# Kernel optimization log

Hardware: AMD Instinct MI355X
Metric: run time of the kernel (lower is better)

## Reference

```python
import jax, jax.numpy as jnp
import numpy as np

NUM_USERS = 100000
NUM_ITEMS = 50000
EMB = 64
N_SOC = 1000000
N_RAT = 1000000
BATCH = 16384
EPS = 1e-8


def setup_inputs() -> dict:
    key = jax.random.key(0)
    ks = jax.random.split(key, 8)
    user_emb = 0.01 * jax.random.normal(ks[0], (NUM_USERS, EMB), jnp.float32)
    item_emb = 0.01 * jax.random.normal(ks[1], (NUM_ITEMS, EMB), jnp.float32)
    users = jax.random.randint(ks[2], (BATCH,), 0, NUM_USERS)
    items = jax.random.randint(ks[3], (BATCH,), 0, NUM_ITEMS)
    social_src = jax.random.randint(ks[4], (N_SOC,), 0, NUM_USERS)
    social_dst = jax.random.randint(ks[5], (N_SOC,), 0, NUM_USERS)
    like_u = jax.random.randint(ks[6], (N_RAT,), 0, NUM_USERS)
    like_i = jax.random.randint(ks[7], (N_RAT,), 0, NUM_ITEMS)
    return {"user_emb": user_emb, "item_emb": item_emb, "users": users,
            "items": items, "social_src": social_src, "social_dst": social_dst,
            "like_u": like_u, "like_i": like_i}


def _deg(idx, num):
    # node degree as float column vector [num, 1]
    return jax.ops.segment_sum(jnp.ones((idx.shape[0],), jnp.float32), idx,
                               num_segments=num)[:, None]


def _seg_mean(msg, idx, num):
    s = jax.ops.segment_sum(msg, idx, num_segments=num)
    cnt = _deg(idx, num)
    return s / jnp.maximum(cnt, 1.0)


def reference(user_emb, item_emb, users, items, social_src, social_dst, like_u, like_i):
    # degree-based self-weights (deg=0 -> 1, deg>0 -> ~0)
    user_deg = _deg(like_u, NUM_USERS)            # out-degree on 'like'
    u_sw = 1.0 - user_deg / (user_deg + EPS)
    item_deg = _deg(like_i, NUM_ITEMS)            # out-degree on 'rev_like'
    i_sw = 1.0 - item_deg / (item_deg + EPS)

    def social_conv(hu):
        # mean aggregation over user->user social edges
        return _seg_mean(hu[social_src], social_dst, NUM_USERS)

    def rating_conv(hu, hi):
        # user <- mean of liked-item embeddings, plus degree-gated self
        new_u = u_sw * hu + _seg_mean(hi[like_i], like_u, NUM_USERS)
        new_i = i_sw * hi + _seg_mean(hu[like_u], like_i, NUM_ITEMS)
        return new_u, new_i

    # layer 1
    soc1 = social_conv(user_emb)
    rat_u1, rat_i1 = rating_conv(user_emb, item_emb)
    u1 = 0.5 * soc1 + 0.5 * rat_u1
    # layer 2 (stacked on per-branch states, as in the torch code)
    soc2 = social_conv(soc1)
    rat_u2, _ = rating_conv(rat_u1, rat_i1)
    u2 = 0.5 * soc2 + 0.5 * rat_u2

    # l_user = [0, 1, 2]
    final_user = user_emb + u1 + u2
    final_item = item_emb

    latest_user = final_user[users]
    latest_item = final_item[items]
    predict = jax.nn.sigmoid(jnp.sum(latest_user * latest_item, axis=1))
    return predict, latest_user, latest_item
```

## Files before the change

### kernel.cpp

```cpp
#include <hip/hip_runtime.h>
#include <hip/hip_bf16.h>

#define NUSERS 100000
#define NITEMS 50000
#define NEDGE  1000000
#define NBATCH 16384
#define CAP_LU 320000
#define EPB    2048
#define NBLK_E ((NEDGE + EPB - 1) / EPB)
#define NBW    3125

#define OFF_GC     0
#define OFF_GB     768
#define OFF_GCUR   1536
#define OFF_BITS   2304
#define OFF_NEED   (OFF_BITS + 3136)
#define OFF_ZEND   (OFF_NEED + NUSERS / 4)
#define OFF_IDEG   OFF_ZEND
#define OFF_UDEG   (OFF_IDEG + NITEMS)
#define OFF_SDEG   (OFF_UDEG + NUSERS)
#define OFF_ISTART (OFF_SDEG + NUSERS)
#define OFF_USTART (OFF_ISTART + NITEMS)
#define OFF_SSTART (OFF_USTART + NUSERS)
#define OFF_PARTLI (OFF_SSTART + NUSERS)
#define OFF_PARTLU (OFF_PARTLI + NEDGE)
#define OFF_PARTSD (OFF_PARTLU + CAP_LU)
#define OFF_UEMBH  OFF_PARTLI
#define OFF_CSRLI  (OFF_UEMBH + NUSERS * 32)
#define OFF_CSRLU  (OFF_CSRLI + NEDGE)
#define OFF_RI1    (OFF_CSRLU + CAP_LU)
#define OFF_SOC1   OFF_CSRLI
#define OFF_CSRSD  (OFF_SOC1 + NUSERS * 32)
#define OFF_RU1C   (OFF_CSRSD + NEDGE)
#define OFF_RU2C   (OFF_RU1C + NBATCH * 32)
#define WS_FLOATS  (OFF_RU2C + NBATCH * 32)

typedef unsigned short u16;

__device__ __forceinline__ float bf2f(u16 h) {
    union { unsigned u; float f; } c; c.u = ((unsigned)h) << 16; return c.f;
}
__device__ __forceinline__ u16 f2bf(float f) {
    union { float f; unsigned u; } c; c.f = f;
    unsigned r = c.u + 0x7fffu + ((c.u >> 16) & 1u);
    return (u16)(r >> 16);
}
__device__ __forceinline__ void acc2(unsigned w, float& a0, float& a1) {
    a0 += bf2f((u16)(w & 0xffff));
    a1 += bf2f((u16)(w >> 16));
}

__global__ void k_slot(const int* __restrict__ users, unsigned* __restrict__ bits,
                       unsigned char* __restrict__ needed) {
    int b = blockIdx.x * blockDim.x + threadIdx.x;
    if (b < NBATCH) {
        int u = users[b];
        atomicOr(&bits[u >> 5], 1u << (u & 31));
        needed[u] = 1;
    }
}

__global__ void k_passA(const int* __restrict__ lu, const int* __restrict__ li,
                        const int* __restrict__ sd, const int* __restrict__ ss,
                        const unsigned* __restrict__ bits, int* __restrict__ gcnt,
                        unsigned char* __restrict__ needed) {
    __shared__ int lc[768];
    __shared__ unsigned sbits[NBW];
    int t = threadIdx.x;
    for (int k = t; k < 768; k += 256) lc[k] = 0;
    for (int k = t; k < NBW; k += 256) sbits[k] = bits[k];
    __syncthreads();
    int base = blockIdx.x * EPB;
    int end = base + EPB; if (end > NEDGE) end = NEDGE;
    for (int e = base + t; e < end; e += 256) {
        int item = li[e], a = lu[e], d = sd[e];
        atomicAdd(&lc[item >> 9], 1);
        if ((sbits[a >> 5] >> (a & 31)) & 1)
            atomicAdd(&lc[256 + (a >> 9)], 1);
        atomicAdd(&lc[512 + (d >> 9)], 1);
        if ((sbits[d >> 5] >> (d & 31)) & 1)
            needed[ss[e]] = 1;
    }
    __syncthreads();
    for (int k = t; k < 768; k += 256)
        if (lc[k]) atomicAdd(&gcnt[k], lc[k]);
}

__global__ void k_passB(const int* __restrict__ gcnt, int* __restrict__ gbase,
                        int* __restrict__ gcur) {
    __shared__ int s[256];
    int t = threadIdx.x;
    for (int j = 0; j < 3; ++j) {
        int v = gcnt[j * 256 + t];
        s[t] = v;
        __syncthreads();
        for (int o = 1; o < 256; o <<= 1) {
            int x = (t >= o) ? s[t - o] : 0;
            __syncthreads();
            s[t] += x;
            __syncthreads();
        }
        int ex = s[t] - v;
        gbase[j * 256 + t] = ex;
        gcur[j * 256 + t] = ex;
        __syncthreads();
    }
}

__global__ void k_passC(const int* __restrict__ lu, const int* __restrict__ li,
                        const int* __restrict__ sd, const int* __restrict__ ss,
                        const unsigned* __restrict__ bits, int* __restrict__ gcur,
                        int* __restrict__ partLI, int* __restrict__ partLU,
                        int* __restrict__ partSD) {
    __shared__ int lc[768];
    __shared__ int go[768];
    __shared__ unsigned sbits[NBW];
    int t = threadIdx.x;
    for (int k = t; k < 768; k += 256) lc[k] = 0;
    for (int k = t; k < NBW; k += 256) sbits[k] = bits[k];
    __syncthreads();
    int base = blockIdx.x * EPB;
    int end = base + EPB; if (end > NEDGE) end = NEDGE;
    unsigned mask = 0;
    int i = 0;
    for (int e = base + t; e < end; e += 256, ++i) {
        int item = li[e], a = lu[e], d = sd[e];
        atomicAdd(&lc[item >> 9], 1);
        if ((sbits[a >> 5] >> (a & 31)) & 1) {
            atomicAdd(&lc[256 + (a >> 9)], 1);
            mask |= (1u << i);
        }
        atomicAdd(&lc[512 + (d >> 9)], 1);
    }
    __syncthreads();
    for (int k = t; k < 768; k += 256) {
        go[k] = lc[k] ? atomicAdd(&gcur[k], lc[k]) : 0;
        lc[k] = 0;
    }
    __syncthreads();
    i = 0;
    for (int e = base + t; e < end; e += 256, ++i) {
        int item = li[e], a = lu[e], d = sd[e], s_ = ss[e];
        int b0 = item >> 9;
        int r0 = atomicAdd(&lc[b0], 1);
        partLI[go[b0] + r0] = (a << 9) | (item & 511);
        if (mask & (1u << i)) {
            int b1 = 256 + (a >> 9);
            int r1 = atomicAdd(&lc[b1], 1);
            partLU[go[b1] + r1] = (item << 9) | (a & 511);
        }
        int b2 = 512 + (d >> 9);
        int r2 = atomicAdd(&lc[b2], 1);
        partSD[go[b2] + r2] = (s_ << 9) | (d & 511);
    }
}

__global__ void k_passD(const int* __restrict__ gcnt, const int* __restrict__ gbase,
                        const int* __restrict__ partLI, const int* __restrict__ partLU,
                        const int* __restrict__ partSD, int* __restrict__ csrli,
                        int* __restrict__ csrlu, int* __restrict__ csrsd,
                        int* __restrict__ ideg, int* __restrict__ udeg,
                        int* __restrict__ sdeg, int* __restrict__ istart,
                        int* __restrict__ ustart, int* __restrict__ sstart) {
    __shared__ int lcnt[512], lstart[512], sb[2][512];
    int t = threadIdx.x;
    int blk = blockIdx.x, list, b;
    const int* part; int* csr; int* deg; int* start; int n;
    if (blk < 196)      { list = 0; b = blk;       part = partLI; csr = csrli; deg = ideg; start = istart; n = NITEMS; }
    else if (blk < 392) { list = 1; b = blk - 196; part = partLU; csr = csrlu; deg = udeg; start = ustart; n = NUSERS; }
    else                { list = 2; b = blk - 392; part = partSD; csr = csrsd; deg = sdeg; start = sstart; n = NUSERS; }
    int base = gbase[list * 256 + b], cnt = gcnt[list * 256 + b];
    int node0 = b << 9;
    int M = n - node0; if (M > 512) M = 512; if (M < 0) M = 0;

    lcnt[t] = 0; lcnt[t + 256] = 0;
    __syncthreads();
    for (int i = t; i < cnt; i += 256) atomicAdd(&lcnt[part[base + i] & 511], 1);
    __syncthreads();
    sb[0][t] = lcnt[t]; sb[0][t + 256] = lcnt[t + 256];
    __syncthreads();
    int pp = 0;
    for (int o = 1; o < 512; o <<= 1) {
        int np = pp ^ 1;
        for (int k = t; k < 512; k += 256) {
            int v = sb[pp][k];
            if (k >= o) v += sb[pp][k - o];
            sb[np][k] = v;
        }
        __syncthreads();
        pp = np;
    }
    for (int k = t; k < 512; k += 256) {
        int ex = sb[pp][k] - lcnt[k];
        lstart[k] = ex;
        if (k < M) { deg[node0 + k] = lcnt[k]; start[node0 + k] = base + ex; }
    }
    __syncthreads();
    lcnt[t] = 0; lcnt[t + 256] = 0;
    __syncthreads();
    for (int i = t; i < cnt; i += 256) {
        int p = part[base + i];
        int nl = p & 511;
        int r = atomicAdd(&lcnt[nl], 1);
        csr[base + lstart[nl] + r] = p >> 9;
    }
}

__global__ void k_cvt(const float* __restrict__ src, u16* __restrict__ dst) {
    int t = blockIdx.x * 256 + threadIdx.x;
    if (t >= NUSERS * 16) return;
    float4 v = ((const float4*)src)[t];
    ushort4 o;
    o.x = f2bf(v.x); o.y = f2bf(v.y); o.z = f2bf(v.z); o.w = f2bf(v.w);
    ((ushort4*)dst)[t] = o;
}

__global__ void k_gather_item(const float* __restrict__ iemb,
                              const unsigned* __restrict__ uh32,
                              const int* __restrict__ csr, const int* __restrict__ istart,
                              const int* __restrict__ ideg, unsigned* __restrict__ ri1) {
    int node = blockIdx.x * 4 + (threadIdx.x >> 6);
    int lane = threadIdx.x & 63;
    if (node >= NITEMS) return;
    int half = lane >> 5, l = lane & 31;
    int j = istart[node], dg = ideg[node], end = j + dg;
    float a0 = 0.f, b0 = 0.f, a1 = 0.f, b1 = 0.f, a2 = 0.f, b2 = 0.f, a3 = 0.f, b3 = 0.f;
    for (; j + 7 < end; j += 8) {
        unsigned w0 = uh32[csr[j     + half] * 32 + l];
        unsigned w1 = uh32[csr[j + 2 + half] * 32 + l];
        unsigned w2 = uh32[csr[j + 4 + half] * 32 + l];
        unsigned w3 = uh32[csr[j + 6 + half] * 32 + l];
        acc2(w0, a0, b0); acc2(w1, a1, b1); acc2(w2, a2, b2); acc2(w3, a3, b3);
    }
    for (; j < end; j += 2) {
        int idx = j + half;
        if (idx < end) { unsigned w = uh32[csr[idx] * 32 + l]; acc2(w, a0, b0); }
    }
    float s0 = (a0 + a1) + (a2 + a3);
    float s1 = (b0 + b1) + (b2 + b3);
    s0 += __shfl_xor(s0, 32);
    s1 += __shfl_xor(s1, 32);
    if (half == 0) {
        float dgf = (float)dg;
        float inv = 1.0f / fmaxf(dgf, 1.0f);
        float sw = 1.0f - dgf / (dgf + 1e-8f);
        float2 ev = ((const float2*)(iemb + node * 64))[l];
        float v0 = sw * ev.x + s0 * inv;
        float v1 = sw * ev.y + s1 * inv;
        ri1[node * 32 + l] = (unsigned)f2bf(v0) | ((unsigned)f2bf(v1) << 16);
    }
}

__global__ void k_batch_rat(const int* __restrict__ users, const float* __restrict__ iemb,
                            const u16* __restrict__ ri1, const int* __restrict__ csr,
                            const int* __restrict__ ustart, const int* __restrict__ udeg,
                            u16* __restrict__ ru1c, u16* __restrict__ ru2c) {
    int b = blockIdx.x * 4 + (threadIdx.x >> 6);
    int lane = threadIdx.x & 63;
    if (b >= NBATCH) return;
    int u = users[b];
    int j = ustart[u], dg = udeg[u], end = j + dg;
    float a1 = 0.f, a2 = 0.f, b1 = 0.f, b2 = 0.f;
    for (; j + 1 < end; j += 2) {
        int i0 = csr[j], i1 = csr[j + 1];
        a1 += iemb[i0 * 64 + lane];
        b1 += iemb[i1 * 64 + lane];
        a2 += bf2f(ri1[i0 * 64 + lane]);
        b2 += bf2f(ri1[i1 * 64 + lane]);
    }
    if (j < end) {
        int i0 = csr[j];
        a1 += iemb[i0 * 64 + lane];
        a2 += bf2f(ri1[i0 * 64 + lane]);
    }
    float inv = 1.0f / fmaxf((float)dg, 1.0f);
    ru1c[b * 64 + lane] = f2bf((a1 + b1) * inv);
    ru2c[b * 64 + lane] = f2bf((a2 + b2) * inv);
}

__global__ void k_gather_soc(const unsigned* __restrict__ uh32,
                             const int* __restrict__ csr, const int* __restrict__ sstart,
                             const int* __restrict__ sdeg,
                             const unsigned char* __restrict__ needed,
                             unsigned* __restrict__ soc1) {
    int node = blockIdx.x * 4 + (threadIdx.x >> 6);
    int lane = threadIdx.x & 63;
    if (node >= NUSERS) return;
    if (!needed[node]) return;
    int half = lane >> 5, l = lane & 31;
    int j = sstart[node], dg = sdeg[node], end = j + dg;
    float a0 = 0.f, b0 = 0.f, a1 = 0.f, b1 = 0.f, a2 = 0.f, b2 = 0.f, a3 = 0.f, b3 = 0.f;
    for (; j + 7 < end; j += 8) {
        unsigned w0 = uh32[csr[j     + half] * 32 + l];
        unsigned w1 = uh32[csr[j + 2 + half] * 32 + l];
        unsigned w2 = uh32[csr[j + 4 + half] * 32 + l];
        unsigned w3 = uh32[csr[j + 6 + half] * 32 + l];
        acc2(w0, a0, b0); acc2(w1, a1, b1); acc2(w2, a2, b2); acc2(w3, a3, b3);
    }
    for (; j < end; j += 2) {
        int idx = j + half;
        if (idx < end) { unsigned w = uh32[csr[idx] * 32 + l]; acc2(w, a0, b0); }
    }
    float s0 = (a0 + a1) + (a2 + a3);
    float s1 = (b0 + b1) + (b2 + b3);
    s0 += __shfl_xor(s0, 32);
    s1 += __shfl_xor(s1, 32);
    if (half == 0) {
        float inv = 1.0f / fmaxf((float)dg, 1.0f);
        soc1[node * 32 + l] = (unsigned)f2bf(s0 * inv) | ((unsigned)f2bf(s1 * inv) << 16);
    }
}

__global__ void k_final(const int* __restrict__ users, const int* __restrict__ items,
                        const float* __restrict__ uemb, const float* __restrict__ iemb,
                        const u16* __restrict__ soc1, const int* __restrict__ csr,
                        const int* __restrict__ sstart, const int* __restrict__ sdeg,
                        const u16* __restrict__ ru1c, const u16* __restrict__ ru2c,
                        const int* __restrict__ udeg, float* __restrict__ out) {
    int b = blockIdx.x * 4 + (threadIdx.x >> 6);
    int d = threadIdx.x & 63;
    if (b >= NBATCH) return;
    int u = users[b], it = items[b];
    int j = sstart[u], dg = sdeg[u], end = j + dg;
    float a = 0.f, a2_ = 0.f;
    for (; j + 1 < end; j += 2) {
        int c0 = csr[j], c1 = csr[j + 1];
        a   += bf2f(soc1[c0 * 64 + d]);
        a2_ += bf2f(soc1[c1 * 64 + d]);
    }
    if (j < end) a += bf2f(soc1[csr[j] * 64 + d]);
    float s2 = (a + a2_) / fmaxf((float)dg, 1.0f);
    float ud = (float)udeg[u];
    float usw = 1.0f - ud / (ud + 1e-8f);
    float ue = uemb[u * 64 + d];
    float s1 = bf2f(soc1[u * 64 + d]);
    float r1 = usw * ue + bf2f(ru1c[b * 64 + d]);
    float r2 = usw * r1 + bf2f(ru2c[b * 64 + d]);
    float fu = ue + 0.5f * (s1 + r1) + 0.5f * (s2 + r2);
    float iv = iemb[it * 64 + d];
    out[NBATCH + b * 64 + d]               = fu;
    out[NBATCH + NBATCH * 64 + b * 64 + d] = iv;
    float p = fu * iv;
    #pragma unroll
    for (int o = 32; o > 0; o >>= 1) p += __shfl_down(p, o);
    if (d == 0) out[b] = 1.0f / (1.0f + __expf(-p));
}

extern "C" void kernel_launch(void* const* d_in, const int* in_sizes, int n_in,
                              void* d_out, int out_size, void* d_ws, size_t ws_size,
                              hipStream_t stream) {
    const float* uemb  = (const float*)d_in[0];
    const float* iemb  = (const float*)d_in[1];
    const int*   users = (const int*)d_in[2];
    const int*   items = (const int*)d_in[3];
    const int*   ssrc  = (const int*)d_in[4];
    const int*   sdst  = (const int*)d_in[5];
    const int*   lu    = (const int*)d_in[6];
    const int*   li    = (const int*)d_in[7];
    float* out = (float*)d_out;

    if (ws_size < (size_t)WS_FLOATS * 4) return;

    int*           W      = (int*)d_ws;
    int*           gcnt   = W + OFF_GC;
    int*           gbase  = W + OFF_GB;
    int*           gcur   = W + OFF_GCUR;
    unsigned*      bits   = (unsigned*)(W + OFF_BITS);
    unsigned char* needed = (unsigned char*)(W + OFF_NEED);
    int*           ideg   = W + OFF_IDEG;
    int*           udeg   = W + OFF_UDEG;
    int*           sdeg   = W + OFF_SDEG;
    int*           istart = W + OFF_ISTART;
    int*           ustart = W + OFF_USTART;
    int*           sstart = W + OFF_SSTART;
    int*           partLI = W + OFF_PARTLI;
    int*           partLU = W + OFF_PARTLU;
    int*           partSD = W + OFF_PARTSD;
    u16*           uembh  = (u16*)(W + OFF_UEMBH);
    int*           csrli  = W + OFF_CSRLI;
    int*           csrlu  = W + OFF_CSRLU;
    int*           csrsd  = W + OFF_CSRSD;
    u16*           ri1    = (u16*)(W + OFF_RI1);
    u16*           soc1   = (u16*)(W + OFF_SOC1);
    u16*           ru1c   = (u16*)(W + OFF_RU1C);
    u16*           ru2c   = (u16*)(W + OFF_RU2C);

    hipMemsetAsync(d_ws, 0, (size_t)OFF_ZEND * 4, stream);

    const int B = 256;

    k_slot<<<(NBATCH + B - 1) / B, B, 0, stream>>>(users, bits, needed);
    k_passA<<<NBLK_E, B, 0, stream>>>(lu, li, sdst, ssrc, bits, gcnt, needed);
    k_passB<<<1, B, 0, stream>>>(gcnt, gbase, gcur);
    k_passC<<<NBLK_E, B, 0, stream>>>(lu, li, sdst, ssrc, bits, gcur,
                                      partLI, partLU, partSD);
    k_passD<<<588, B, 0, stream>>>(gcnt, gbase, partLI, partLU, partSD,
                                   csrli, csrlu, csrsd, ideg, udeg, sdeg,
                                   istart, ustart, sstart);

    k_cvt<<<(NUSERS * 16 + B - 1) / B, B, 0, stream>>>(uemb, uembh);

    k_gather_item<<<(NITEMS + 3) / 4, B, 0, stream>>>(iemb, (const unsigned*)uembh,
                                                      csrli, istart, ideg, (unsigned*)ri1);
    k_batch_rat<<<(NBATCH + 3) / 4, B, 0, stream>>>(users, iemb, ri1, csrlu, ustart,
                                                    udeg, ru1c, ru2c);
    k_gather_soc<<<(NUSERS + 3) / 4, B, 0, stream>>>((const unsigned*)uembh, csrsd,
                                                     sstart, sdeg, needed, (unsigned*)soc1);

    k_final<<<(NBATCH + 3) / 4, B, 0, stream>>>(users, items, uemb, iemb, soc1,
                                                csrsd, sstart, sdeg, ru1c, ru2c, udeg, out);
}
```

Baseline: 294.8 us.

## Use grid-stride gather kernels with wave-wide CSR index preload and paired nodes

```diff
diff --git a/kernel.cpp b/kernel.cpp
--- a/kernel.cpp
+++ b/kernel.cpp
@@ -9,6 +9,7 @@
 #define EPB    2048
 #define NBLK_E ((NEDGE + EPB - 1) / EPB)
 #define NBW    3125
+#define GGRID  2048
 
 #define OFF_GC     0
 #define OFF_GB     768
@@ -219,35 +220,64 @@
                               const unsigned* __restrict__ uh32,
                               const int* __restrict__ csr, const int* __restrict__ istart,
                               const int* __restrict__ ideg, unsigned* __restrict__ ri1) {
-    int node = blockIdx.x * 4 + (threadIdx.x >> 6);
     int lane = threadIdx.x & 63;
-    if (node >= NITEMS) return;
+    int wid  = blockIdx.x * 4 + (threadIdx.x >> 6);
+    int nw   = gridDim.x * 4;
     int half = lane >> 5, l = lane & 31;
-    int j = istart[node], dg = ideg[node], end = j + dg;
-    float a0 = 0.f, b0 = 0.f, a1 = 0.f, b1 = 0.f, a2 = 0.f, b2 = 0.f, a3 = 0.f, b3 = 0.f;
-    for (; j + 7 < end; j += 8) {
-        unsigned w0 = uh32[csr[j     + half] * 32 + l];
-        unsigned w1 = uh32[csr[j + 2 + half] * 32 + l];
-        unsigned w2 = uh32[csr[j + 4 + half] * 32 + l];
-        unsigned w3 = uh32[csr[j + 6 + half] * 32 + l];
-        acc2(w0, a0, b0); acc2(w1, a1, b1); acc2(w2, a2, b2); acc2(w3, a3, b3);
-    }
-    for (; j < end; j += 2) {
-        int idx = j + half;
-        if (idx < end) { unsigned w = uh32[csr[idx] * 32 + l]; acc2(w, a0, b0); }
-    }
-    float s0 = (a0 + a1) + (a2 + a3);
-    float s1 = (b0 + b1) + (b2 + b3);
-    s0 += __shfl_xor(s0, 32);
-    s1 += __shfl_xor(s1, 32);
-    if (half == 0) {
-        float dgf = (float)dg;
-        float inv = 1.0f / fmaxf(dgf, 1.0f);
-        float sw = 1.0f - dgf / (dgf + 1e-8f);
-        float2 ev = ((const float2*)(iemb + node * 64))[l];
-        float v0 = sw * ev.x + s0 * inv;
-        float v1 = sw * ev.y + s1 * inv;
-        ri1[node * 32 + l] = (unsigned)f2bf(v0) | ((unsigned)f2bf(v1) << 16);
+    for (int nA = wid * 2; nA < NITEMS; nA += nw * 2) {
+        int nB = nA + 1;
+        int jA = istart[nA], dA = ideg[nA];
+        int jB = istart[nB], dB = ideg[nB];
+        int cA = (lane < dA) ? csr[jA + lane] : 0;
+        int cB = (lane < dB) ? csr[jB + lane] : 0;
+        float a0=0.f,b0=0.f,a1=0.f,b1=0.f,a2=0.f,b2=0.f,a3=0.f,b3=0.f;
+        float e0a=0.f,f0a=0.f,e1a=0.f,f1a=0.f,e2a=0.f,f2a=0.f,e3a=0.f,f3a=0.f;
+        int kmA = dA < 64 ? dA : 64;
+        int kmB = dB < 64 ? dB : 64;
+        int km = kmA > kmB ? kmA : kmB;
+        for (int k = 0; k < km; k += 8) {
+            int q0 = k + half, q1 = k + 2 + half, q2 = k + 4 + half, q3 = k + 6 + half;
+            int rA0 = __shfl(cA, q0), rA1 = __shfl(cA, q1);
+            int rA2 = __shfl(cA, q2), rA3 = __shfl(cA, q3);
+            int rB0 = __shfl(cB, q0), rB1 = __shfl(cB, q1);
+            int rB2 = __shfl(cB, q2), rB3 = __shfl(cB, q3);
+            if (q0 < kmA) acc2(uh32[rA0 * 32 + l], a0, b0);
+            if (q1 < kmA) acc2(uh32[rA1 * 32 + l], a1, b1);
+            if (q2 < kmA) acc2(uh32[rA2 * 32 + l], a2, b2);
+            if (q3 < kmA) acc2(uh32[rA3 * 32 + l], a3, b3);
+            if (q0 < kmB) acc2(uh32[rB0 * 32 + l], e0a, f0a);
+            if (q1 < kmB) acc2(uh32[rB1 * 32 + l], e1a, f1a);
+            if (q2 < kmB) acc2(uh32[rB2 * 32 + l], e2a, f2a);
+            if (q3 < kmB) acc2(uh32[rB3 * 32 + l], e3a, f3a);
+        }
+        for (int j = jA + 64; j < jA + dA; j += 2) {
+            int idx = j + half;
+            if (idx < jA + dA) acc2(uh32[csr[idx] * 32 + l], a0, b0);
+        }
+        for (int j = jB + 64; j < jB + dB; j += 2) {
+            int idx = j + half;
+            if (idx < jB + dB) acc2(uh32[csr[idx] * 32 + l], e0a, f0a);
+        }
+        float sA0 = (a0 + a1) + (a2 + a3);
+        float sA1 = (b0 + b1) + (b2 + b3);
+        float sB0 = (e0a + e1a) + (e2a + e3a);
+        float sB1 = (f0a + f1a) + (f2a + f3a);
+        sA0 += __shfl_xor(sA0, 32); sA1 += __shfl_xor(sA1, 32);
+        sB0 += __shfl_xor(sB0, 32); sB1 += __shfl_xor(sB1, 32);
+        if (half == 0) {
+            float dgf = (float)dA;
+            float inv = 1.0f / fmaxf(dgf, 1.0f);
+            float sw = 1.0f - dgf / (dgf + 1e-8f);
+            float2 ev = ((const float2*)(iemb + nA * 64))[l];
+            ri1[nA * 32 + l] = (unsigned)f2bf(sw * ev.x + sA0 * inv)
+                             | ((unsigned)f2bf(sw * ev.y + sA1 * inv) << 16);
+            float dgg = (float)dB;
+            float inv2 = 1.0f / fmaxf(dgg, 1.0f);
+            float sw2 = 1.0f - dgg / (dgg + 1e-8f);
+            float2 ev2 = ((const float2*)(iemb + nB * 64))[l];
+            ri1[nB * 32 + l] = (unsigned)f2bf(sw2 * ev2.x + sB0 * inv2)
+                             | ((unsigned)f2bf(sw2 * ev2.y + sB1 * inv2) << 16);
+        }
     }
 }
 
@@ -255,27 +285,31 @@
                             const u16* __restrict__ ri1, const int* __restrict__ csr,
                             const int* __restrict__ ustart, const int* __restrict__ udeg,
                             u16* __restrict__ ru1c, u16* __restrict__ ru2c) {
-    int b = blockIdx.x * 4 + (threadIdx.x >> 6);
     int lane = threadIdx.x & 63;
-    if (b >= NBATCH) return;
-    int u = users[b];
-    int j = ustart[u], dg = udeg[u], end = j + dg;
-    float a1 = 0.f, a2 = 0.f, b1 = 0.f, b2 = 0.f;
-    for (; j + 1 < end; j += 2) {
-        int i0 = csr[j], i1 = csr[j + 1];
-        a1 += iemb[i0 * 64 + lane];
-        b1 += iemb[i1 * 64 + lane];
-        a2 += bf2f(ri1[i0 * 64 + lane]);
-        b2 += bf2f(ri1[i1 * 64 + lane]);
-    }
-    if (j < end) {
-        int i0 = csr[j];
-        a1 += iemb[i0 * 64 + lane];
-        a2 += bf2f(ri1[i0 * 64 + lane]);
-    }
-    float inv = 1.0f / fmaxf((float)dg, 1.0f);
-    ru1c[b * 64 + lane] = f2bf((a1 + b1) * inv);
-    ru2c[b * 64 + lane] = f2bf((a2 + b2) * inv);
+    int wid  = blockIdx.x * 4 + (threadIdx.x >> 6);
+    int nw   = gridDim.x * 4;
+    for (int b = wid; b < NBATCH; b += nw) {
+        int u = users[b];
+        int j0 = ustart[u], dg = udeg[u];
+        int cv = (lane < dg) ? csr[j0 + lane] : 0;
+        float p0=0.f,p1=0.f,p2=0.f,p3=0.f, q0=0.f,q1=0.f,q2=0.f,q3=0.f;
+        int km = dg < 64 ? dg : 64;
+        for (int k = 0; k < km; k += 4) {
+            int i0 = __shfl(cv, k),     i1 = __shfl(cv, k + 1);
+            int i2 = __shfl(cv, k + 2), i3 = __shfl(cv, k + 3);
+            p0 += iemb[i0 * 64 + lane]; q0 += bf2f(ri1[i0 * 64 + lane]);
+            if (k + 1 < km) { p1 += iemb[i1 * 64 + lane]; q1 += bf2f(ri1[i1 * 64 + lane]); }
+            if (k + 2 < km) { p2 += iemb[i2 * 64 + lane]; q2 += bf2f(ri1[i2 * 64 + lane]); }
+            if (k + 3 < km) { p3 += iemb[i3 * 64 + lane]; q3 += bf2f(ri1[i3 * 64 + lane]); }
+        }
+        for (int j = j0 + 64; j < j0 + dg; ++j) {
+            int i0 = csr[j];
+            p0 += iemb[i0 * 64 + lane]; q0 += bf2f(ri1[i0 * 64 + lane]);
+        }
+        float inv = 1.0f / fmaxf((float)dg, 1.0f);
+        ru1c[b * 64 + lane] = f2bf(((p0 + p1) + (p2 + p3)) * inv);
+        ru2c[b * 64 + lane] = f2bf(((q0 + q1) + (q2 + q3)) * inv);
+    }
 }
 
 __global__ void k_gather_soc(const unsigned* __restrict__ uh32,
@@ -283,31 +317,65 @@
                              const int* __restrict__ sdeg,
                              const unsigned char* __restrict__ needed,
                              unsigned* __restrict__ soc1) {
-    int node = blockIdx.x * 4 + (threadIdx.x >> 6);
     int lane = threadIdx.x & 63;
-    if (node >= NUSERS) return;
-    if (!needed[node]) return;
+    int wid  = blockIdx.x * 4 + (threadIdx.x >> 6);
+    int nw   = gridDim.x * 4;
     int half = lane >> 5, l = lane & 31;
-    int j = sstart[node], dg = sdeg[node], end = j + dg;
-    float a0 = 0.f, b0 = 0.f, a1 = 0.f, b1 = 0.f, a2 = 0.f, b2 = 0.f, a3 = 0.f, b3 = 0.f;
-    for (; j + 7 < end; j += 8) {
-        unsigned w0 = uh32[csr[j     + half] * 32 + l];
-        unsigned w1 = uh32[csr[j + 2 + half] * 32 + l];
-        unsigned w2 = uh32[csr[j + 4 + half] * 32 + l];
-        unsigned w3 = uh32[csr[j + 6 + half] * 32 + l];
-        acc2(w0, a0, b0); acc2(w1, a1, b1); acc2(w2, a2, b2); acc2(w3, a3, b3);
-    }
-    for (; j < end; j += 2) {
-        int idx = j + half;
-        if (idx < end) { unsigned w = uh32[csr[idx] * 32 + l]; acc2(w, a0, b0); }
-    }
-    float s0 = (a0 + a1) + (a2 + a3);
-    float s1 = (b0 + b1) + (b2 + b3);
-    s0 += __shfl_xor(s0, 32);
-    s1 += __shfl_xor(s1, 32);
-    if (half == 0) {
-        float inv = 1.0f / fmaxf((float)dg, 1.0f);
-        soc1[node * 32 + l] = (unsigned)f2bf(s0 * inv) | ((unsigned)f2bf(s1 * inv) << 16);
+    for (int nA = wid * 2; nA < NUSERS; nA += nw * 2) {
+        int nB = nA + 1;
+        unsigned short nd = *(const unsigned short*)(needed + nA);
+        if (!nd) continue;
+        int needA = nd & 0xff, needB = nd >> 8;
+        int jA = sstart[nA], dA = needA ? sdeg[nA] : 0;
+        int jB = sstart[nB], dB = needB ? sdeg[nB] : 0;
+        int cA = (lane < dA) ? csr[jA + lane] : 0;
+        int cB = (lane < dB) ? csr[jB + lane] : 0;
+        float a0=0.f,b0=0.f,a1=0.f,b1=0.f,a2=0.f,b2=0.f,a3=0.f,b3=0.f;
+        float e0a=0.f,f0a=0.f,e1a=0.f,f1a=0.f,e2a=0.f,f2a=0.f,e3a=0.f,f3a=0.f;
+        int kmA = dA < 64 ? dA : 64;
+        int kmB = dB < 64 ? dB : 64;
+        int km = kmA > kmB ? kmA : kmB;
+        for (int k = 0; k < km; k += 8) {
+            int q0 = k + half, q1 = k + 2 + half, q2 = k + 4 + half, q3 = k + 6 + half;
+            int rA0 = __shfl(cA, q0), rA1 = __shfl(cA, q1);
+            int rA2 = __shfl(cA, q2), rA3 = __shfl(cA, q3);
+            int rB0 = __shfl(cB, q0), rB1 = __shfl(cB, q1);
+            int rB2 = __shfl(cB, q2), rB3 = __shfl(cB, q3);
+            if (q0 < kmA) acc2(uh32[rA0 * 32 + l], a0, b0);
+            if (q1 < kmA) acc2(uh32[rA1 * 32 + l], a1, b1);
+            if (q2 < kmA) acc2(uh32[rA2 * 32 + l], a2, b2);
+            if (q3 < kmA) acc2(uh32[rA3 * 32 + l], a3, b3);
+            if (q0 < kmB) acc2(uh32[rB0 * 32 + l], e0a, f0a);
+            if (q1 < kmB) acc2(uh32[rB1 * 32 + l], e1a, f1a);
+            if (q2 < kmB) acc2(uh32[rB2 * 32 + l], e2a, f2a);
+            if (q3 < kmB) acc2(uh32[rB3 * 32 + l], e3a, f3a);
+        }
+        for (int j = jA + 64; j < jA + dA; j += 2) {
+            int idx = j + half;
+            if (idx < jA + dA) acc2(uh32[csr[idx] * 32 + l], a0, b0);
+        }
+        for (int j = jB + 64; j < jB + dB; j += 2) {
+            int idx = j + half;
+            if (idx < jB + dB) acc2(uh32[csr[idx] * 32 + l], e0a, f0a);
+        }
+        float sA0 = (a0 + a1) + (a2 + a3);
+        float sA1 = (b0 + b1) + (b2 + b3);
+        float sB0 = (e0a + e1a) + (e2a + e3a);
+        float sB1 = (f0a + f1a) + (f2a + f3a);
+        sA0 += __shfl_xor(sA0, 32); sA1 += __shfl_xor(sA1, 32);
+        sB0 += __shfl_xor(sB0, 32); sB1 += __shfl_xor(sB1, 32);
+        if (half == 0) {
+            if (needA) {
+                float inv = 1.0f / fmaxf((float)dA, 1.0f);
+                soc1[nA * 32 + l] = (unsigned)f2bf(sA0 * inv)
+                                  | ((unsigned)f2bf(sA1 * inv) << 16);
+            }
+            if (needB) {
+                float inv = 1.0f / fmaxf((float)dB, 1.0f);
+                soc1[nB * 32 + l] = (unsigned)f2bf(sB0 * inv)
+                                  | ((unsigned)f2bf(sB1 * inv) << 16);
+            }
+        }
     }
 }
 
@@ -317,33 +385,41 @@
                         const int* __restrict__ sstart, const int* __restrict__ sdeg,
                         const u16* __restrict__ ru1c, const u16* __restrict__ ru2c,
                         const int* __restrict__ udeg, float* __restrict__ out) {
-    int b = blockIdx.x * 4 + (threadIdx.x >> 6);
-    int d = threadIdx.x & 63;
-    if (b >= NBATCH) return;
-    int u = users[b], it = items[b];
-    int j = sstart[u], dg = sdeg[u], end = j + dg;
-    float a = 0.f, a2_ = 0.f;
-    for (; j + 1 < end; j += 2) {
-        int c0 = csr[j], c1 = csr[j + 1];
-        a   += bf2f(soc1[c0 * 64 + d]);
-        a2_ += bf2f(soc1[c1 * 64 + d]);
-    }
-    if (j < end) a += bf2f(soc1[csr[j] * 64 + d]);
-    float s2 = (a + a2_) / fmaxf((float)dg, 1.0f);
-    float ud = (float)udeg[u];
-    float usw = 1.0f - ud / (ud + 1e-8f);
-    float ue = uemb[u * 64 + d];
-    float s1 = bf2f(soc1[u * 64 + d]);
-    float r1 = usw * ue + bf2f(ru1c[b * 64 + d]);
-    float r2 = usw * r1 + bf2f(ru2c[b * 64 + d]);
-    float fu = ue + 0.5f * (s1 + r1) + 0.5f * (s2 + r2);
-    float iv = iemb[it * 64 + d];
-    out[NBATCH + b * 64 + d]               = fu;
-    out[NBATCH + NBATCH * 64 + b * 64 + d] = iv;
-    float p = fu * iv;
-    #pragma unroll
-    for (int o = 32; o > 0; o >>= 1) p += __shfl_down(p, o);
-    if (d == 0) out[b] = 1.0f / (1.0f + __expf(-p));
+    int d   = threadIdx.x & 63;
+    int wid = blockIdx.x * 4 + (threadIdx.x >> 6);
+    int nw  = gridDim.x * 4;
+    for (int b = wid; b < NBATCH; b += nw) {
+        int u = users[b], it = items[b];
+        int j0 = sstart[u], dg = sdeg[u];
+        int cv = (d < dg) ? csr[j0 + d] : 0;
+        float s0=0.f, s1a=0.f, s2a=0.f, s3a=0.f;
+        int km = dg < 64 ? dg : 64;
+        for (int k = 0; k < km; k += 4) {
+            int c0 = __shfl(cv, k),     c1 = __shfl(cv, k + 1);
+            int c2 = __shfl(cv, k + 2), c3 = __shfl(cv, k + 3);
+            s0 += bf2f(soc1[c0 * 64 + d]);
+            if (k + 1 < km) s1a += bf2f(soc1[c1 * 64 + d]);
+            if (k + 2 < km) s2a += bf2f(soc1[c2 * 64 + d]);
+            if (k + 3 < km) s3a += bf2f(soc1[c3 * 64 + d]);
+        }
+        for (int j = j0 + 64; j < j0 + dg; ++j)
+            s0 += bf2f(soc1[csr[j] * 64 + d]);
+        float s2 = ((s0 + s1a) + (s2a + s3a)) / fmaxf((float)dg, 1.0f);
+        float ud = (float)udeg[u];
+        float usw = 1.0f - ud / (ud + 1e-8f);
+        float ue = uemb[u * 64 + d];
+        float s1 = bf2f(soc1[u * 64 + d]);
+        float r1 = usw * ue + bf2f(ru1c[b * 64 + d]);
+        float r2 = usw * r1 + bf2f(ru2c[b * 64 + d]);
+        float fu = ue + 0.5f * (s1 + r1) + 0.5f * (s2 + r2);
+        float iv = iemb[it * 64 + d];
+        out[NBATCH + b * 64 + d]               = fu;
+        out[NBATCH + NBATCH * 64 + b * 64 + d] = iv;
+        float p = fu * iv;
+        #pragma unroll
+        for (int o = 32; o > 0; o >>= 1) p += __shfl_down(p, o);
+        if (d == 0) out[b] = 1.0f / (1.0f + __expf(-p));
+    }
 }
 
 extern "C" void kernel_launch(void* const* d_in, const int* in_sizes, int n_in,
@@ -400,13 +476,13 @@
 
     k_cvt<<<(NUSERS * 16 + B - 1) / B, B, 0, stream>>>(uemb, uembh);
 
-    k_gather_item<<<(NITEMS + 3) / 4, B, 0, stream>>>(iemb, (const unsigned*)uembh,
-                                                      csrli, istart, ideg, (unsigned*)ri1);
-    k_batch_rat<<<(NBATCH + 3) / 4, B, 0, stream>>>(users, iemb, ri1, csrlu, ustart,
-                                                    udeg, ru1c, ru2c);
-    k_gather_soc<<<(NUSERS + 3) / 4, B, 0, stream>>>((const unsigned*)uembh, csrsd,
-                                                     sstart, sdeg, needed, (unsigned*)soc1);
-
-    k_final<<<(NBATCH + 3) / 4, B, 0, stream>>>(users, items, uemb, iemb, soc1,
-                                                csrsd, sstart, sdeg, ru1c, ru2c, udeg, out);
-}
+    k_gather_item<<<GGRID, B, 0, stream>>>(iemb, (const unsigned*)uembh,
+                                           csrli, istart, ideg, (unsigned*)ri1);
+    k_batch_rat<<<GGRID, B, 0, stream>>>(users, iemb, ri1, csrlu, ustart,
+                                         udeg, ru1c, ru2c);
+    k_gather_soc<<<GGRID, B, 0, stream>>>((const unsigned*)uembh, csrsd,
+                                          sstart, sdeg, needed, (unsigned*)soc1);
+
+    k_final<<<GGRID, B, 0, stream>>>(users, items, uemb, iemb, soc1,
+                                     csrsd, sstart, sdeg, ru1c, ru2c, udeg, out);
+}
```

Measured after the change: 296.8 us. No clear change (+0.7%).
